# Performance work log

Measured on AMD Instinct MI355X. Metric: run time of the kernel, lower is better.

Reference implementation:

```python
import jax, jax.numpy as jnp
import numpy as np

B, C, D = 16384, 512, 512
EXT = 2
H = C * EXT
TAU = 1.0          # temperature_train
STEP = 0.05        # langevin_step_size
NOISE = 0.1        # langevin_noise
STEPS = 32         # langevin_steps


def setup_inputs() -> dict:
    key = jax.random.key(0)
    ks = jax.random.split(key, 8)
    s_in = 1.0 / np.sqrt(D)
    s_h = 1.0 / np.sqrt(H)
    return {
        'x': jax.random.normal(ks[0], (B, D), jnp.float32),
        'vanilla_components': jnp.abs(jax.random.normal(ks[1], (C, D), jnp.float32) * 0.1),
        'e_sp': jax.random.normal(ks[2], (C * D,), jnp.float32) * 0.1,
        'W1e': jax.random.normal(ks[3], (D, H), jnp.float32) * s_in,
        'b1e': jnp.zeros((H,), jnp.float32),
        'W2e': jax.random.normal(ks[4], (H, C), jnp.float32) * s_h,
        'b2e': jnp.zeros((C,), jnp.float32),
        'W1r': jax.random.normal(ks[5], (D, H), jnp.float32) * s_in,
        'b1r': jnp.zeros((H,), jnp.float32),
        'W2r': jax.random.normal(ks[6], (H, C), jnp.float32) * s_h,
        'b2r': jnp.zeros((C,), jnp.float32),
    }


def _langevin_gate(e, key):
    """Langevin MCMC on latent u with quadratic energy E(u)=0.5||u||^2 + <e,u>.
    Returns selection probability sigmoid(-u/tau)."""
    def step(u, k):
        grad = u + e  # dE/du
        u = u - STEP * grad + NOISE * jax.random.normal(k, u.shape, u.dtype)
        return u, None
    u, _ = jax.lax.scan(step, jnp.zeros_like(e), jax.random.split(key, STEPS))
    return jax.nn.sigmoid(-u / TAU)


def reference(x, vanilla_components, e_sp, W1e, b1e, W2e, b2e, W1r, b1r, W2r, b2r):
    k1, k2 = jax.random.split(jax.random.key(42))
    # non-negative components
    comps = jnp.abs(vanilla_components)  # [C, D]
    # fixed energy-based sparsity mask over component entries
    p_sp = _langevin_gate(e_sp, k1).reshape(C, D)
    comps = comps * p_sp
    # dynamic per-sample component selection energies via MLP
    h = jax.nn.relu(x @ W1e + b1e)          # [B, H]
    e_dyn = h @ W2e + b2e                   # [B, C]
    gate = _langevin_gate(e_dyn, k2)        # [B, C] soft gates (train mode)
    hr = jax.nn.relu(x @ W1r + b1r)         # [B, H]
    conc = (hr @ W2r + b2r) * gate          # [B, C]
    # aggregate: (concentration * components).sum over components -> [B, D]
    return conc @ comps
```

## Files before the change

kernel.cpp:

```cpp
#include <hip/hip_runtime.h>
#include <hip/hip_bf16.h>
#include <stdint.h>

#define Bn 16384
#define Cn 512
#define Dn 512
#define Hn 1024

#define A32 0.80628851f

typedef __attribute__((ext_vector_type(8))) short bf16x8;
typedef __attribute__((ext_vector_type(4))) float f32x4;
typedef __attribute__((ext_vector_type(2))) float f32x2;

__device__ __forceinline__ ushort f2bf(float f) {
  uint32_t u = __float_as_uint(f);
  return (ushort)((u + 0x7fffu + ((u >> 16) & 1u)) >> 16);
}
__device__ __forceinline__ float b2f(ushort u) {
  return __uint_as_float((uint32_t)u << 16);
}

__device__ __forceinline__ uint32_t rotl32(uint32_t v, int s) {
  return __builtin_rotateleft32(v, (uint32_t)s);
}

__device__ __forceinline__ void threefry2x32(uint32_t k0, uint32_t k1,
                                             uint32_t x0, uint32_t x1,
                                             uint32_t& o0, uint32_t& o1) {
  const uint32_t k2 = k0 ^ k1 ^ 0x1BD11BDAu;
  x0 += k0; x1 += k1;
#define TFR(r) { x0 += x1; x1 = rotl32(x1, (r)); x1 ^= x0; }
  TFR(13) TFR(15) TFR(26) TFR(6)   x0 += k1; x1 += k2 + 1u;
  TFR(17) TFR(29) TFR(16) TFR(24)  x0 += k2; x1 += k0 + 2u;
  TFR(13) TFR(15) TFR(26) TFR(6)   x0 += k0; x1 += k1 + 3u;
  TFR(17) TFR(29) TFR(16) TFR(24)  x0 += k1; x1 += k2 + 4u;
  TFR(13) TFR(15) TFR(26) TFR(6)   x0 += k2; x1 += k0 + 5u;
#undef TFR
  o0 = x0; o1 = x1;
}

__device__ __forceinline__ float bits_to_normal(uint32_t bits) {
  float f = __uint_as_float((bits >> 9) | 0x3f800000u) - 1.0f;
  float x = f * 2.0f - 0x1.fffffep-1f;
  float w = -__logf(1.0f - x * x);
  float p;
  if (w < 5.0f) {
    w -= 2.5f;
    p =            2.81022636e-08f;
    p = fmaf(p, w, 3.43273939e-07f);
    p = fmaf(p, w, -3.5233877e-06f);
    p = fmaf(p, w, -4.39150654e-06f);
    p = fmaf(p, w, 0.00021858087f);
    p = fmaf(p, w, -0.00125372503f);
    p = fmaf(p, w, -0.00417768164f);
    p = fmaf(p, w, 0.246640727f);
    p = fmaf(p, w, 1.50140941f);
  } else {
    w = sqrtf(w) - 3.0f;
    p =            -0.000200214257f;
    p = fmaf(p, w, 0.000100950558f);
    p = fmaf(p, w, 0.00134934322f);
    p = fmaf(p, w, -0.00367342844f);
    p = fmaf(p, w, 0.00573950773f);
    p = fmaf(p, w, -0.0076224613f);
    p = fmaf(p, w, 0.00943887047f);
    p = fmaf(p, w, 1.00167406f);
    p = fmaf(p, w, 2.83297682f);
  }
  return 0x1.6a09e6p+0f * (p * x);
}

__global__ void k_setup_keys(uint32_t* __restrict__ keys) {
  if (threadIdx.x != 0 || blockIdx.x != 0) return;
  uint32_t k1w0, k1w1, k2w0, k2w1;
  threefry2x32(0u, 42u, 0u, 0u, k1w0, k1w1);
  threefry2x32(0u, 42u, 0u, 1u, k2w0, k2w1);
  for (uint32_t t = 0; t < 32; ++t) {
    uint32_t w0, w1;
    threefry2x32(k1w0, k1w1, 0u, t, w0, w1);
    keys[2 * t] = w0; keys[2 * t + 1] = w1;
    threefry2x32(k2w0, k2w1, 0u, t, w0, w1);
    keys[64 + 2 * t] = w0; keys[64 + 2 * t + 1] = w1;
  }
}

__global__ __launch_bounds__(256) void k_transpose_cvt(
    const float* __restrict__ in, ushort* __restrict__ out, int NO, int KO) {
  int o = blockIdx.x * 256 + threadIdx.x;
  int n = o / KO, k = o % KO;
  out[o] = f2bf(in[(size_t)k * NO + n]);
}

__global__ __launch_bounds__(256) void k_cvt_x(const float* __restrict__ in,
                                               ushort* __restrict__ out) {
  int i = (blockIdx.x * 256 + threadIdx.x) * 4;
  float4 v = *(const float4*)(in + i);
  *(ushort4*)(out + i) = make_ushort4(f2bf(v.x), f2bf(v.y), f2bf(v.z), f2bf(v.w));
}


__device__ __forceinline__ void gemm_tile_bf(
    const ushort* __restrict__ A, const ushort* __restrict__ WT,
    const float* __restrict__ bias, ushort* __restrict__ Out, int g,
    ushort As[128][40], ushort Bs[128][40]) {
  const int n0 = (g & 7) * 128, m0 = (g >> 3) * 128;
  const int t = threadIdx.x;
  const int srow = t >> 1, skb = (t & 1) << 4;
  const ushort* Ap = A  + (size_t)(m0 + srow) * Dn + skb;
  const ushort* Bp = WT + (size_t)(n0 + srow) * Dn + skb;
  const int wave = t >> 6, lane = t & 63;
  const int wm = (wave >> 1) << 6, wn = (wave & 1) << 6;
  const int quad = lane >> 4, l15 = lane & 15;

  f32x4 acc[4][4] = {};
  for (int k0 = 0; k0 < Dn; k0 += 32) {
    uint4 a0 = *(const uint4*)(Ap + k0);
    uint4 a1 = *(const uint4*)(Ap + k0 + 8);
    uint4 b0 = *(const uint4*)(Bp + k0);
    uint4 b1 = *(const uint4*)(Bp + k0 + 8);
    *(uint4*)&As[srow][skb] = a0; *(uint4*)&As[srow][skb + 8] = a1;
    *(uint4*)&Bs[srow][skb] = b0; *(uint4*)&Bs[srow][skb + 8] = b1;
    __syncthreads();
    bf16x8 af[4], bfr[4];
#pragma unroll
    for (int i = 0; i < 4; ++i) {
      af[i] = *(const bf16x8*)&As[wm + i * 16 + l15][quad * 8];
      bfr[i] = *(const bf16x8*)&Bs[wn + i * 16 + l15][quad * 8];
    }
#pragma unroll
    for (int i = 0; i < 4; ++i)
#pragma unroll
      for (int j = 0; j < 4; ++j)
        acc[i][j] = __builtin_amdgcn_mfma_f32_16x16x32_bf16(af[i], bfr[j],
                                                            acc[i][j], 0, 0, 0);
    __syncthreads();
  }
#pragma unroll
  for (int i = 0; i < 4; ++i)
#pragma unroll
    for (int j = 0; j < 4; ++j) {
      const int col = n0 + wn + j * 16 + l15;
      const float bv = bias[col];
#pragma unroll
      for (int r = 0; r < 4; ++r) {
        const int row = m0 + wm + i * 16 + quad * 4 + r;
        Out[(size_t)row * Hn + col] = f2bf(fmaxf(acc[i][j][r] + bv, 0.0f));
      }
    }
}

__device__ __forceinline__ void smask_block(
    const float* __restrict__ vc, const float* __restrict__ e_sp,
    const uint32_t* __restrict__ keys, ushort* __restrict__ compsT, int g) {
  uint32_t j = (uint32_t)g * 256 + threadIdx.x;
  uint32_t c = j & (Cn - 1), d = j >> 9;
  uint32_t ridx = c * Dn + d;
  float e = e_sp[ridx];
  float u = 0.0f;
#pragma unroll 1
  for (int t = 0; t < 32; ++t) {
    uint32_t o0, o1;
    threefry2x32(keys[2 * t], keys[2 * t + 1], 0u, ridx, o0, o1);
    float n = bits_to_normal(o0 ^ o1);
    u = (u - 0.05f * (u + e)) + 0.1f * n;
  }
  float gt = 1.0f / (1.0f + __expf(u));
  compsT[j] = f2bf(fabsf(vc[ridx]) * gt);
}

__device__ __forceinline__ void zdyn_block(
    const uint32_t* __restrict__ keys, ushort* __restrict__ Z, uint32_t rb) {
  const uint32_t j0 = (rb * 256u + threadIdx.x) * 4u;
  f32x2 zA = {0.0f, 0.0f}, zB = {0.0f, 0.0f};
  const f32x2 C95 = {0.95f, 0.95f};
  const f32x2 CNS = {0.14142135f, 0.14142135f};
#pragma unroll 2
  for (int t = 0; t < 32; ++t) {
    const uint32_t K0 = keys[2 * t], K1 = keys[2 * t + 1];
    const uint32_t KX = K0 ^ K1 ^ 0x1BD11BDAu;
    uint32_t a0 = K0, a1 = K0, a2 = K0, a3 = K0;
    uint32_t b0 = K1 + j0, b1 = K1 + j0 + 1u, b2 = K1 + j0 + 2u,
             b3 = K1 + j0 + 3u;
#define R4(r)                                                            \
    a0 += b0; a1 += b1; a2 += b2; a3 += b3;                              \
    b0 = rotl32(b0, r); b1 = rotl32(b1, r);                              \
    b2 = rotl32(b2, r); b3 = rotl32(b3, r);                              \
    b0 ^= a0; b1 ^= a1; b2 ^= a2; b3 ^= a3;
#define I4(p, q)                                                         \
    a0 += (p); a1 += (p); a2 += (p); a3 += (p);                          \
    b0 += (q); b1 += (q); b2 += (q); b3 += (q);
    R4(13) R4(15) R4(26) R4(6)  I4(K1, KX + 1u)
    R4(17) R4(29) R4(16) R4(24) I4(KX, K0 + 2u)
    R4(13) R4(15) R4(26) R4(6)  I4(K0, K1 + 3u)
    R4(17) R4(29) R4(16) R4(24) I4(K1, KX + 4u)
    R4(13) R4(15) R4(26) R4(6)  I4(KX, K0 + 5u)
#undef R4
#undef I4
    float X0, W0, X1, W1, X2, W2, X3, W3;
#define WPREP(s, xo, wo) {                                               \
    float f_ = __uint_as_float(((s) >> 9) | 0x3f800000u) - 1.0f;         \
    xo = f_ * 2.0f - 0x1.fffffep-1f;                                     \
    wo = fminf(-__logf(fmaf(-xo, xo, 1.0f)), 5.0f) - 2.5f; }
    WPREP(a0 ^ b0, X0, W0)
    WPREP(a1 ^ b1, X1, W1)
    WPREP(a2 ^ b2, X2, W2)
    WPREP(a3 ^ b3, X3, W3)
#undef WPREP
    f32x2 xA = {X0, X1}, wA = {W0, W1};
    f32x2 xB = {X2, X3}, wB = {W2, W3};
#define POLY(w, x, zacc) {                                               \
    f32x2 p_ = (f32x2){2.81022636e-08f, 2.81022636e-08f};                \
    p_ = p_ * (w) + (f32x2){3.43273939e-07f, 3.43273939e-07f};           \
    p_ = p_ * (w) + (f32x2){-3.5233877e-06f, -3.5233877e-06f};           \
    p_ = p_ * (w) + (f32x2){-4.39150654e-06f, -4.39150654e-06f};         \
    p_ = p_ * (w) + (f32x2){0.00021858087f, 0.00021858087f};             \
    p_ = p_ * (w) + (f32x2){-0.00125372503f, -0.00125372503f};           \
    p_ = p_ * (w) + (f32x2){-0.00417768164f, -0.00417768164f};           \
    p_ = p_ * (w) + (f32x2){0.246640727f, 0.246640727f};                 \
    p_ = p_ * (w) + (f32x2){1.50140941f, 1.50140941f};                   \
    zacc = C95 * (zacc) + (p_ * (x)) * CNS; }
    POLY(wA, xA, zA)
    POLY(wB, xB, zB)
#undef POLY
  }
  *(ushort4*)(Z + j0) =
      make_ushort4(f2bf(zA.x), f2bf(zA.y), f2bf(zB.x), f2bf(zB.y));
}

__global__ __launch_bounds__(256) void k_mega(
    const ushort* __restrict__ x_bf,
    const ushort* __restrict__ W1eT, const float* __restrict__ b1e,
    ushort* __restrict__ h,
    const ushort* __restrict__ W1rT, const float* __restrict__ b1r,
    ushort* __restrict__ hr,
    const float* __restrict__ vc, const float* __restrict__ e_sp,
    const uint32_t* __restrict__ keys, ushort* __restrict__ compsT,
    ushort* __restrict__ Zdyn) {
  __shared__ ushort As[128][40];
  __shared__ ushort Bs[128][40];
  const uint32_t bx = blockIdx.x;
  const uint32_t group = bx / 11u, pos = bx % 11u;
  if (pos == 0u)
    gemm_tile_bf(x_bf, W1eT, b1e, h, (int)group, As, Bs);
  else if (pos == 1u)
    gemm_tile_bf(x_bf, W1rT, b1r, hr, (int)group, As, Bs);
  else if (pos == 2u)
    smask_block(vc, e_sp, keys, compsT, (int)group);
  else
    zdyn_block(keys + 64, Zdyn, group * 8u + (pos - 3u));
}

__global__ __launch_bounds__(256) void k_dgemm(
    const ushort* __restrict__ h, const ushort* __restrict__ W2eT,
    const float* __restrict__ b2e,
    const ushort* __restrict__ hr, const ushort* __restrict__ W2rT,
    const float* __restrict__ b2r,
    ushort* __restrict__ Zconc) {
  __shared__ ushort As[128][40];
  __shared__ ushort Bs[128][40];
  const int t = threadIdx.x;
  const int m0 = blockIdx.y * 128, n0 = blockIdx.x * 128;
  const int srow = t >> 1, skb = (t & 1) << 4;
  const int wave = t >> 6, lane = t & 63;
  const int wm = (wave >> 1) << 6, wn = (wave & 1) << 6;
  const int quad = lane >> 4, l15 = lane & 15;

  const ushort* Ap = h    + (size_t)(m0 + srow) * Hn + skb;
  const ushort* Bp = W2eT + (size_t)(n0 + srow) * Hn + skb;
  f32x4 acc[4][4] = {};
  for (int k0 = 0; k0 < Hn; k0 += 32) {
    uint4 a0 = *(const uint4*)(Ap + k0);
    uint4 a1 = *(const uint4*)(Ap + k0 + 8);
    uint4 b0 = *(const uint4*)(Bp + k0);
    uint4 b1 = *(const uint4*)(Bp + k0 + 8);
    *(uint4*)&As[srow][skb] = a0; *(uint4*)&As[srow][skb + 8] = a1;
    *(uint4*)&Bs[srow][skb] = b0; *(uint4*)&Bs[srow][skb + 8] = b1;
    __syncthreads();
    bf16x8 af[4], bfr[4];
#pragma unroll
    for (int i = 0; i < 4; ++i) {
      af[i] = *(const bf16x8*)&As[wm + i * 16 + l15][quad * 8];
      bfr[i] = *(const bf16x8*)&Bs[wn + i * 16 + l15][quad * 8];
    }
#pragma unroll
    for (int i = 0; i < 4; ++i)
#pragma unroll
      for (int j = 0; j < 4; ++j)
        acc[i][j] = __builtin_amdgcn_mfma_f32_16x16x32_bf16(af[i], bfr[j],
                                                            acc[i][j], 0, 0, 0);
    __syncthreads();
  }
  float g[4][4][4];
#pragma unroll
  for (int i = 0; i < 4; ++i)
#pragma unroll
    for (int j = 0; j < 4; ++j) {
      const int col = n0 + wn + j * 16 + l15;
      const float bv = b2e[col];
#pragma unroll
      for (int r = 0; r < 4; ++r) {
        const int row = m0 + wm + i * 16 + quad * 4 + r;
        float e = acc[i][j][r] + bv;
        float z = b2f(Zconc[(size_t)row * Cn + col]);
        g[i][j][r] = 1.0f / (1.0f + __expf(z - A32 * e));
        acc[i][j][r] = 0.0f;
      }
    }
  Ap = hr   + (size_t)(m0 + srow) * Hn + skb;
  Bp = W2rT + (size_t)(n0 + srow) * Hn + skb;
  for (int k0 = 0; k0 < Hn; k0 += 32) {
    uint4 a0 = *(const uint4*)(Ap + k0);
    uint4 a1 = *(const uint4*)(Ap + k0 + 8);
    uint4 b0 = *(const uint4*)(Bp + k0);
    uint4 b1 = *(const uint4*)(Bp + k0 + 8);
    __syncthreads();
    *(uint4*)&As[srow][skb] = a0; *(uint4*)&As[srow][skb + 8] = a1;
    *(uint4*)&Bs[srow][skb] = b0; *(uint4*)&Bs[srow][skb + 8] = b1;
    __syncthreads();
    bf16x8 af[4], bfr[4];
#pragma unroll
    for (int i = 0; i < 4; ++i) {
      af[i] = *(const bf16x8*)&As[wm + i * 16 + l15][quad * 8];
      bfr[i] = *(const bf16x8*)&Bs[wn + i * 16 + l15][quad * 8];
    }
#pragma unroll
    for (int i = 0; i < 4; ++i)
#pragma unroll
      for (int j = 0; j < 4; ++j)
        acc[i][j] = __builtin_amdgcn_mfma_f32_16x16x32_bf16(af[i], bfr[j],
                                                            acc[i][j], 0, 0, 0);
  }
#pragma unroll
  for (int i = 0; i < 4; ++i)
#pragma unroll
    for (int j = 0; j < 4; ++j) {
      const int col = n0 + wn + j * 16 + l15;
      const float bv = b2r[col];
#pragma unroll
      for (int r = 0; r < 4; ++r) {
        const int row = m0 + wm + i * 16 + quad * 4 + r;
        Zconc[(size_t)row * Cn + col] = f2bf((acc[i][j][r] + bv) * g[i][j][r]);
      }
    }
}

__global__ __launch_bounds__(256) void k_gemm_out(
    const ushort* __restrict__ A, const ushort* __restrict__ WT,
    float* __restrict__ Out) {
  __shared__ ushort As[128][40];
  __shared__ ushort Bs[128][40];
  const int t = threadIdx.x;
  const int m0 = blockIdx.y * 128, n0 = blockIdx.x * 128;
  const int srow = t >> 1, skb = (t & 1) << 4;
  const ushort* Ap = A  + (size_t)(m0 + srow) * Cn + skb;
  const ushort* Bp = WT + (size_t)(n0 + srow) * Cn + skb;
  const int wave = t >> 6, lane = t & 63;
  const int wm = (wave >> 1) << 6, wn = (wave & 1) << 6;
  const int quad = lane >> 4, l15 = lane & 15;

  f32x4 acc[4][4] = {};
  for (int k0 = 0; k0 < Cn; k0 += 32) {
    uint4 a0 = *(const uint4*)(Ap + k0);
    uint4 a1 = *(const uint4*)(Ap + k0 + 8);
    uint4 b0 = *(const uint4*)(Bp + k0);
    uint4 b1 = *(const uint4*)(Bp + k0 + 8);
    *(uint4*)&As[srow][skb] = a0; *(uint4*)&As[srow][skb + 8] = a1;
    *(uint4*)&Bs[srow][skb] = b0; *(uint4*)&Bs[srow][skb + 8] = b1;
    __syncthreads();
    bf16x8 af[4], bfr[4];
#pragma unroll
    for (int i = 0; i < 4; ++i) {
      af[i] = *(const bf16x8*)&As[wm + i * 16 + l15][quad * 8];
      bfr[i] = *(const bf16x8*)&Bs[wn + i * 16 + l15][quad * 8];
    }
#pragma unroll
    for (int i = 0; i < 4; ++i)
#pragma unroll
      for (int j = 0; j < 4; ++j)
        acc[i][j] = __builtin_amdgcn_mfma_f32_16x16x32_bf16(af[i], bfr[j],
                                                            acc[i][j], 0, 0, 0);
    __syncthreads();
  }
#pragma unroll
  for (int i = 0; i < 4; ++i)
#pragma unroll
    for (int j = 0; j < 4; ++j) {
      const int col = n0 + wn + j * 16 + l15;
#pragma unroll
      for (int r = 0; r < 4; ++r) {
        const int row = m0 + wm + i * 16 + quad * 4 + r;
        Out[(size_t)row * Dn + col] = acc[i][j][r];
      }
    }
}

extern "C" void kernel_launch(void* const* d_in, const int* in_sizes, int n_in,
                              void* d_out, int out_size, void* d_ws, size_t ws_size,
                              hipStream_t stream) {
  const float* x    = (const float*)d_in[0];
  const float* vc   = (const float*)d_in[1];
  const float* e_sp = (const float*)d_in[2];
  const float* W1e  = (const float*)d_in[3];
  const float* b1e  = (const float*)d_in[4];
  const float* W2e  = (const float*)d_in[5];
  const float* b2e  = (const float*)d_in[6];
  const float* W1r  = (const float*)d_in[7];
  const float* b1r  = (const float*)d_in[8];
  const float* W2r  = (const float*)d_in[9];
  const float* b2r  = (const float*)d_in[10];
  float* out = (float*)d_out;

  char* ws = (char*)d_ws;
  uint32_t* keys = (uint32_t*)ws;
  ushort* W1eT   = (ushort*)(ws + (1u << 12));
  ushort* W2eT   = (ushort*)(ws + (1u << 12) + (1u << 20));
  ushort* W1rT   = (ushort*)(ws + (1u << 12) + (2u << 20));
  ushort* W2rT   = (ushort*)(ws + (1u << 12) + (3u << 20));
  ushort* compsT = (ushort*)(ws + (1u << 12) + (4u << 20));
  ushort* Zdyn   = (ushort*)(ws + (8u << 20));
  ushort* h_bf   = (ushort*)(ws + (24u << 20));
  ushort* hr_bf  = (ushort*)(ws + (56u << 20));
  ushort* x_bf   = (ushort*)d_out;

  k_setup_keys<<<1, 64, 0, stream>>>(keys);
  k_cvt_x<<<(Bn * Dn / 4) / 256, 256, 0, stream>>>(x, x_bf);
  k_transpose_cvt<<<(Dn * Hn) / 256, 256, 0, stream>>>(W1e, W1eT, Hn, Dn);
  k_transpose_cvt<<<(Hn * Cn) / 256, 256, 0, stream>>>(W2e, W2eT, Cn, Hn);
  k_transpose_cvt<<<(Dn * Hn) / 256, 256, 0, stream>>>(W1r, W1rT, Hn, Dn);
  k_transpose_cvt<<<(Hn * Cn) / 256, 256, 0, stream>>>(W2r, W2rT, Cn, Hn);
  k_mega<<<11264, 256, 0, stream>>>(x_bf, W1eT, b1e, h_bf, W1rT, b1r, hr_bf,
                                    vc, e_sp, keys, compsT, Zdyn);
  k_dgemm<<<dim3(Cn / 128, Bn / 128), 256, 0, stream>>>(
      h_bf, W2eT, b2e, hr_bf, W2rT, b2r, Zdyn);
  k_gemm_out<<<dim3(Dn / 128, Bn / 128), 256, 0, stream>>>(Zdyn, compsT, out);
}
```

Before: 852.3 us.

## Bake Threefry key schedule into compile-time constants and split smask kernel

The per-step Threefry keys are now computed at compile time with constexpr and folded into the RNG loops as immediates, which removes the key-setup kernel and the per-step key loads. The sparsity-mask Langevin work moves into its own kernel. The dynamic-gate noise blocks switch from four elements per thread to one, so the mega kernel grows to more blocks with 32 zdyn blocks per GEMM tile pair. Fully unrolling 32 steps with constant keys lengthens the code and may raise register pressure. Lower per-thread ILP in zdyn is traded for more parallelism.

```diff
diff --git a/kernel.cpp b/kernel.cpp
--- a/kernel.cpp
+++ b/kernel.cpp
@@ -21,23 +21,53 @@
   return __uint_as_float((uint32_t)u << 16);
 }
 
+constexpr uint32_t crotl(uint32_t v, int s) {
+  return (v << s) | (v >> (32 - s));
+}
+struct TFOut { uint32_t w0, w1; };
+constexpr TFOut ctf(uint32_t k0, uint32_t k1, uint32_t x0, uint32_t x1) {
+  const uint32_t ks[3] = {k0, k1, k0 ^ k1 ^ 0x1BD11BDAu};
+  const int rot[8] = {13, 15, 26, 6, 17, 29, 16, 24};
+  uint32_t a = x0 + k0, b = x1 + k1;
+  for (int g = 0; g < 5; ++g) {
+    for (int i = 0; i < 4; ++i) {
+      int r = rot[(g & 1) * 4 + i];
+      a += b; b = crotl(b, r); b ^= a;
+    }
+    a += ks[(g + 1) % 3];
+    b += ks[(g + 2) % 3] + (uint32_t)(g + 1);
+  }
+  return {a, b};
+}
+struct KeySched { uint32_t s[64]; uint32_t d[64]; };
+constexpr KeySched make_keys() {
+  KeySched K{};
+  TFOut k1 = ctf(0u, 42u, 0u, 0u);
+  TFOut k2 = ctf(0u, 42u, 0u, 1u);
+  for (uint32_t t = 0; t < 32; ++t) {
+    TFOut ws = ctf(k1.w0, k1.w1, 0u, t);
+    K.s[2 * t] = ws.w0; K.s[2 * t + 1] = ws.w1;
+    TFOut wd = ctf(k2.w0, k2.w1, 0u, t);
+    K.d[2 * t] = wd.w0; K.d[2 * t + 1] = wd.w1;
+  }
+  return K;
+}
+constexpr KeySched KS = make_keys();
+
 __device__ __forceinline__ uint32_t rotl32(uint32_t v, int s) {
   return __builtin_rotateleft32(v, (uint32_t)s);
 }
-
-__device__ __forceinline__ void threefry2x32(uint32_t k0, uint32_t k1,
-                                             uint32_t x0, uint32_t x1,
-                                             uint32_t& o0, uint32_t& o1) {
-  const uint32_t k2 = k0 ^ k1 ^ 0x1BD11BDAu;
-  x0 += k0; x1 += k1;
-#define TFR(r) { x0 += x1; x1 = rotl32(x1, (r)); x1 ^= x0; }
-  TFR(13) TFR(15) TFR(26) TFR(6)   x0 += k1; x1 += k2 + 1u;
-  TFR(17) TFR(29) TFR(16) TFR(24)  x0 += k2; x1 += k0 + 2u;
-  TFR(13) TFR(15) TFR(26) TFR(6)   x0 += k0; x1 += k1 + 3u;
-  TFR(17) TFR(29) TFR(16) TFR(24)  x0 += k1; x1 += k2 + 4u;
-  TFR(13) TFR(15) TFR(26) TFR(6)   x0 += k2; x1 += k0 + 5u;
-#undef TFR
-  o0 = x0; o1 = x1;
+__device__ __forceinline__ uint32_t tf_xor(uint32_t K0, uint32_t K1,
+                                           uint32_t KX, uint32_t j) {
+  uint32_t a = K0, b = K1 + j;
+#define TR(r) { a += b; b = rotl32(b, (r)); b ^= a; }
+  TR(13) TR(15) TR(26) TR(6)   a += K1; b += KX + 1u;
+  TR(17) TR(29) TR(16) TR(24)  a += KX; b += K0 + 2u;
+  TR(13) TR(15) TR(26) TR(6)   a += K0; b += K1 + 3u;
+  TR(17) TR(29) TR(16) TR(24)  a += K1; b += KX + 4u;
+  TR(13) TR(15) TR(26) TR(6)   a += KX; b += K0 + 5u;
+#undef TR
+  return a ^ b;
 }
 
 __device__ __forceinline__ float bits_to_normal(uint32_t bits) {
@@ -71,34 +101,56 @@
   return 0x1.6a09e6p+0f * (p * x);
 }
 
-__global__ void k_setup_keys(uint32_t* __restrict__ keys) {
-  if (threadIdx.x != 0 || blockIdx.x != 0) return;
-  uint32_t k1w0, k1w1, k2w0, k2w1;
-  threefry2x32(0u, 42u, 0u, 0u, k1w0, k1w1);
-  threefry2x32(0u, 42u, 0u, 1u, k2w0, k2w1);
-  for (uint32_t t = 0; t < 32; ++t) {
-    uint32_t w0, w1;
-    threefry2x32(k1w0, k1w1, 0u, t, w0, w1);
-    keys[2 * t] = w0; keys[2 * t + 1] = w1;
-    threefry2x32(k2w0, k2w1, 0u, t, w0, w1);
-    keys[64 + 2 * t] = w0; keys[64 + 2 * t + 1] = w1;
-  }
-}
-
-__global__ __launch_bounds__(256) void k_transpose_cvt(
-    const float* __restrict__ in, ushort* __restrict__ out, int NO, int KO) {
-  int o = blockIdx.x * 256 + threadIdx.x;
-  int n = o / KO, k = o % KO;
-  out[o] = f2bf(in[(size_t)k * NO + n]);
-}
-
-__global__ __launch_bounds__(256) void k_cvt_x(const float* __restrict__ in,
-                                               ushort* __restrict__ out) {
-  int i = (blockIdx.x * 256 + threadIdx.x) * 4;
-  float4 v = *(const float4*)(in + i);
-  *(ushort4*)(out + i) = make_ushort4(f2bf(v.x), f2bf(v.y), f2bf(v.z), f2bf(v.w));
-}
-
+__global__ __launch_bounds__(256) void k_smask(
+    const float* __restrict__ vc, const float* __restrict__ e_sp,
+    ushort* __restrict__ compsT) {
+  uint32_t jj = blockIdx.x * 256 + threadIdx.x;
+  uint32_t c = jj & (Cn - 1), d = jj >> 9;
+  uint32_t ridx = c * Dn + d;
+  float e = e_sp[ridx];
+  float u = 0.0f;
+#pragma unroll
+  for (int t = 0; t < 32; ++t) {
+    const uint32_t K0 = KS.s[2 * t], K1 = KS.s[2 * t + 1];
+    uint32_t s = tf_xor(K0, K1, K0 ^ K1 ^ 0x1BD11BDAu, ridx);
+    float n = bits_to_normal(s);
+    u = (u - 0.05f * (u + e)) + 0.1f * n;
+  }
+  float gt = 1.0f / (1.0f + __expf(u));
+  compsT[jj] = f2bf(fabsf(vc[ridx]) * gt);
+}
+
+__device__ __forceinline__ void zdyn_block(ushort* __restrict__ Z, uint32_t rb) {
+  const uint32_t j = rb * 256u + threadIdx.x;
+  float z = 0.0f;
+#pragma unroll
+  for (int t = 0; t < 32; t += 2) {
+    const uint32_t Ka0 = KS.d[2 * t],     Ka1 = KS.d[2 * t + 1];
+    const uint32_t Kb0 = KS.d[2 * t + 2], Kb1 = KS.d[2 * t + 3];
+    uint32_t s0 = tf_xor(Ka0, Ka1, Ka0 ^ Ka1 ^ 0x1BD11BDAu, j);
+    uint32_t s1 = tf_xor(Kb0, Kb1, Kb0 ^ Kb1 ^ 0x1BD11BDAu, j);
+    float f0 = __uint_as_float((s0 >> 9) | 0x3f800000u) - 1.0f;
+    float f1 = __uint_as_float((s1 >> 9) | 0x3f800000u) - 1.0f;
+    float x0 = f0 * 2.0f - 0x1.fffffep-1f;
+    float x1 = f1 * 2.0f - 0x1.fffffep-1f;
+    float w0 = fminf(-__logf(fmaf(-x0, x0, 1.0f)), 5.0f) - 2.5f;
+    float w1 = fminf(-__logf(fmaf(-x1, x1, 1.0f)), 5.0f) - 2.5f;
+    f32x2 X = {x0, x1}, W = {w0, w1};
+    f32x2 P = {2.81022636e-08f, 2.81022636e-08f};
+    P = __builtin_elementwise_fma(P, W, (f32x2){3.43273939e-07f, 3.43273939e-07f});
+    P = __builtin_elementwise_fma(P, W, (f32x2){-3.5233877e-06f, -3.5233877e-06f});
+    P = __builtin_elementwise_fma(P, W, (f32x2){-4.39150654e-06f, -4.39150654e-06f});
+    P = __builtin_elementwise_fma(P, W, (f32x2){0.00021858087f, 0.00021858087f});
+    P = __builtin_elementwise_fma(P, W, (f32x2){-0.00125372503f, -0.00125372503f});
+    P = __builtin_elementwise_fma(P, W, (f32x2){-0.00417768164f, -0.00417768164f});
+    P = __builtin_elementwise_fma(P, W, (f32x2){0.246640727f, 0.246640727f});
+    P = __builtin_elementwise_fma(P, W, (f32x2){1.50140941f, 1.50140941f});
+    f32x2 Q = (P * X) * (f32x2){0.14142135f, 0.14142135f};
+    z = fmaf(0.95f, z, Q.x);
+    z = fmaf(0.95f, z, Q.y);
+  }
+  Z[j] = f2bf(z);
+}
 
 __device__ __forceinline__ void gemm_tile_bf(
     const ushort* __restrict__ A, const ushort* __restrict__ WT,
@@ -150,105 +202,37 @@
     }
 }
 
-__device__ __forceinline__ void smask_block(
-    const float* __restrict__ vc, const float* __restrict__ e_sp,
-    const uint32_t* __restrict__ keys, ushort* __restrict__ compsT, int g) {
-  uint32_t j = (uint32_t)g * 256 + threadIdx.x;
-  uint32_t c = j & (Cn - 1), d = j >> 9;
-  uint32_t ridx = c * Dn + d;
-  float e = e_sp[ridx];
-  float u = 0.0f;
-#pragma unroll 1
-  for (int t = 0; t < 32; ++t) {
-    uint32_t o0, o1;
-    threefry2x32(keys[2 * t], keys[2 * t + 1], 0u, ridx, o0, o1);
-    float n = bits_to_normal(o0 ^ o1);
-    u = (u - 0.05f * (u + e)) + 0.1f * n;
-  }
-  float gt = 1.0f / (1.0f + __expf(u));
-  compsT[j] = f2bf(fabsf(vc[ridx]) * gt);
-}
-
-__device__ __forceinline__ void zdyn_block(
-    const uint32_t* __restrict__ keys, ushort* __restrict__ Z, uint32_t rb) {
-  const uint32_t j0 = (rb * 256u + threadIdx.x) * 4u;
-  f32x2 zA = {0.0f, 0.0f}, zB = {0.0f, 0.0f};
-  const f32x2 C95 = {0.95f, 0.95f};
-  const f32x2 CNS = {0.14142135f, 0.14142135f};
-#pragma unroll 2
-  for (int t = 0; t < 32; ++t) {
-    const uint32_t K0 = keys[2 * t], K1 = keys[2 * t + 1];
-    const uint32_t KX = K0 ^ K1 ^ 0x1BD11BDAu;
-    uint32_t a0 = K0, a1 = K0, a2 = K0, a3 = K0;
-    uint32_t b0 = K1 + j0, b1 = K1 + j0 + 1u, b2 = K1 + j0 + 2u,
-             b3 = K1 + j0 + 3u;
-#define R4(r)                                                            \
-    a0 += b0; a1 += b1; a2 += b2; a3 += b3;                              \
-    b0 = rotl32(b0, r); b1 = rotl32(b1, r);                              \
-    b2 = rotl32(b2, r); b3 = rotl32(b3, r);                              \
-    b0 ^= a0; b1 ^= a1; b2 ^= a2; b3 ^= a3;
-#define I4(p, q)                                                         \
-    a0 += (p); a1 += (p); a2 += (p); a3 += (p);                          \
-    b0 += (q); b1 += (q); b2 += (q); b3 += (q);
-    R4(13) R4(15) R4(26) R4(6)  I4(K1, KX + 1u)
-    R4(17) R4(29) R4(16) R4(24) I4(KX, K0 + 2u)
-    R4(13) R4(15) R4(26) R4(6)  I4(K0, K1 + 3u)
-    R4(17) R4(29) R4(16) R4(24) I4(K1, KX + 4u)
-    R4(13) R4(15) R4(26) R4(6)  I4(KX, K0 + 5u)
-#undef R4
-#undef I4
-    float X0, W0, X1, W1, X2, W2, X3, W3;
-#define WPREP(s, xo, wo) {                                               \
-    float f_ = __uint_as_float(((s) >> 9) | 0x3f800000u) - 1.0f;         \
-    xo = f_ * 2.0f - 0x1.fffffep-1f;                                     \
-    wo = fminf(-__logf(fmaf(-xo, xo, 1.0f)), 5.0f) - 2.5f; }
-    WPREP(a0 ^ b0, X0, W0)
-    WPREP(a1 ^ b1, X1, W1)
-    WPREP(a2 ^ b2, X2, W2)
-    WPREP(a3 ^ b3, X3, W3)
-#undef WPREP
-    f32x2 xA = {X0, X1}, wA = {W0, W1};
-    f32x2 xB = {X2, X3}, wB = {W2, W3};
-#define POLY(w, x, zacc) {                                               \
-    f32x2 p_ = (f32x2){2.81022636e-08f, 2.81022636e-08f};                \
-    p_ = p_ * (w) + (f32x2){3.43273939e-07f, 3.43273939e-07f};           \
-    p_ = p_ * (w) + (f32x2){-3.5233877e-06f, -3.5233877e-06f};           \
-    p_ = p_ * (w) + (f32x2){-4.39150654e-06f, -4.39150654e-06f};         \
-    p_ = p_ * (w) + (f32x2){0.00021858087f, 0.00021858087f};             \
-    p_ = p_ * (w) + (f32x2){-0.00125372503f, -0.00125372503f};           \
-    p_ = p_ * (w) + (f32x2){-0.00417768164f, -0.00417768164f};           \
-    p_ = p_ * (w) + (f32x2){0.246640727f, 0.246640727f};                 \
-    p_ = p_ * (w) + (f32x2){1.50140941f, 1.50140941f};                   \
-    zacc = C95 * (zacc) + (p_ * (x)) * CNS; }
-    POLY(wA, xA, zA)
-    POLY(wB, xB, zB)
-#undef POLY
-  }
-  *(ushort4*)(Z + j0) =
-      make_ushort4(f2bf(zA.x), f2bf(zA.y), f2bf(zB.x), f2bf(zB.y));
-}
-
-__global__ __launch_bounds__(256) void k_mega(
+__global__ __launch_bounds__(256) void k_mega2(
     const ushort* __restrict__ x_bf,
     const ushort* __restrict__ W1eT, const float* __restrict__ b1e,
     ushort* __restrict__ h,
     const ushort* __restrict__ W1rT, const float* __restrict__ b1r,
     ushort* __restrict__ hr,
-    const float* __restrict__ vc, const float* __restrict__ e_sp,
-    const uint32_t* __restrict__ keys, ushort* __restrict__ compsT,
     ushort* __restrict__ Zdyn) {
   __shared__ ushort As[128][40];
   __shared__ ushort Bs[128][40];
   const uint32_t bx = blockIdx.x;
-  const uint32_t group = bx / 11u, pos = bx % 11u;
+  const uint32_t group = bx / 34u, pos = bx % 34u;
   if (pos == 0u)
     gemm_tile_bf(x_bf, W1eT, b1e, h, (int)group, As, Bs);
   else if (pos == 1u)
     gemm_tile_bf(x_bf, W1rT, b1r, hr, (int)group, As, Bs);
-  else if (pos == 2u)
-    smask_block(vc, e_sp, keys, compsT, (int)group);
   else
-    zdyn_block(keys + 64, Zdyn, group * 8u + (pos - 3u));
+    zdyn_block(Zdyn, group * 32u + (pos - 2u));
+}
+
+__global__ __launch_bounds__(256) void k_cvt_x(const float* __restrict__ in,
+                                               ushort* __restrict__ out) {
+  int i = (blockIdx.x * 256 + threadIdx.x) * 4;
+  float4 v = *(const float4*)(in + i);
+  *(ushort4*)(out + i) = make_ushort4(f2bf(v.x), f2bf(v.y), f2bf(v.z), f2bf(v.w));
+}
+
+__global__ __launch_bounds__(256) void k_transpose_cvt(
+    const float* __restrict__ in, ushort* __restrict__ out, int NO, int KO) {
+  int o = blockIdx.x * 256 + threadIdx.x;
+  int n = o / KO, k = o % KO;
+  out[o] = f2bf(in[(size_t)k * NO + n]);
 }
 
 __global__ __launch_bounds__(256) void k_dgemm(
@@ -412,7 +396,6 @@
   float* out = (float*)d_out;
 
   char* ws = (char*)d_ws;
-  uint32_t* keys = (uint32_t*)ws;
   ushort* W1eT   = (ushort*)(ws + (1u << 12));
   ushort* W2eT   = (ushort*)(ws + (1u << 12) + (1u << 20));
   ushort* W1rT   = (ushort*)(ws + (1u << 12) + (2u << 20));
@@ -423,14 +406,14 @@
   ushort* hr_bf  = (ushort*)(ws + (56u << 20));
   ushort* x_bf   = (ushort*)d_out;
 
-  k_setup_keys<<<1, 64, 0, stream>>>(keys);
   k_cvt_x<<<(Bn * Dn / 4) / 256, 256, 0, stream>>>(x, x_bf);
   k_transpose_cvt<<<(Dn * Hn) / 256, 256, 0, stream>>>(W1e, W1eT, Hn, Dn);
   k_transpose_cvt<<<(Hn * Cn) / 256, 256, 0, stream>>>(W2e, W2eT, Cn, Hn);
   k_transpose_cvt<<<(Dn * Hn) / 256, 256, 0, stream>>>(W1r, W1rT, Hn, Dn);
   k_transpose_cvt<<<(Hn * Cn) / 256, 256, 0, stream>>>(W2r, W2rT, Cn, Hn);
-  k_mega<<<11264, 256, 0, stream>>>(x_bf, W1eT, b1e, h_bf, W1rT, b1r, hr_bf,
-                                    vc, e_sp, keys, compsT, Zdyn);
+  k_smask<<<(Cn * Dn) / 256, 256, 0, stream>>>(vc, e_sp, compsT);
+  k_mega2<<<34816, 256, 0, stream>>>(x_bf, W1eT, b1e, h_bf, W1rT, b1r, hr_bf,
+                                     Zdyn);
   k_dgemm<<<dim3(Cn / 128, Bn / 128), 256, 0, stream>>>(
       h_bf, W2eT, b2e, hr_bf, W2rT, b2r, Zdyn);
   k_gemm_out<<<dim3(Dn / 128, Bn / 128), 256, 0, stream>>>(Zdyn, compsT, out);
```

Measured after the change: 878.8 us. +3.1%, slower.
